# Kernel optimization log

Hardware: AMD Instinct MI355X
Metric: run time of the kernel (lower is better)

## Reference

```python
import jax, jax.numpy as jnp
import numpy as np

MAX_BOXES = 20
IOU_THRESHOLD = 0.1
SCORE_THRESHOLD = 0.3
NUM_CLASSES = 80
N_BOXES = 10647  # YOLOv3 @416: 3*(13^2 + 26^2 + 52^2)


def setup_inputs() -> dict:
    key = jax.random.key(0)
    k1, k2, k3 = jax.random.split(key, 3)
    # boxes in [y1, x1, y2, x2] format (what tf.image.non_max_suppression expects)
    mins = jax.random.uniform(k1, (N_BOXES, 2), minval=0.0, maxval=400.0)
    sizes = jax.random.uniform(k2, (N_BOXES, 2), minval=10.0, maxval=120.0)
    boxes = jnp.concatenate([mins, mins + sizes], axis=1)  # [N,4]
    box_scores = jax.random.uniform(k3, (N_BOXES, NUM_CLASSES))  # [N,C]
    return {"boxes": boxes, "box_scores": box_scores}


def _iou_one_vs_all(box, boxes):
    # box [4], boxes [N,4], format [y1,x1,y2,x2]
    tl = jnp.maximum(box[:2], boxes[:, :2])
    br = jnp.minimum(box[2:], boxes[:, 2:])
    inter = jnp.prod(jnp.clip(br - tl, 0.0), axis=1)
    area1 = jnp.prod(box[2:] - box[:2])
    areas = jnp.prod(boxes[:, 2:] - boxes[:, :2], axis=1)
    union = area1 + areas - inter
    return jnp.where(union > 0, inter / union, 0.0)


def _nms_single_class(boxes, scores):
    """Greedy NMS for one class. Returns padded ([MAX_BOXES] int32 indices, [MAX_BOXES] bool valid).
    Matches tf.image.non_max_suppression semantics (suppress when IoU > threshold),
    applied after the score_threshold mask (invalid scores set to -inf)."""
    n = scores.shape[0]
    s0 = jnp.where(scores >= SCORE_THRESHOLD, scores, -jnp.inf)

    def body(i, state):
        s, idxs, valid = state
        j = jnp.argmax(s)
        ok = s[j] > -jnp.inf
        iou = _iou_one_vs_all(boxes[j], boxes)  # [N]
        suppress = (iou > IOU_THRESHOLD) | (jnp.arange(n) == j)
        s = jnp.where(ok & suppress, -jnp.inf, s)
        idxs = idxs.at[i].set(jnp.where(ok, j, -1).astype(jnp.int32))
        valid = valid.at[i].set(ok)
        return (s, idxs, valid)

    init = (s0, jnp.full((MAX_BOXES,), -1, jnp.int32), jnp.zeros((MAX_BOXES,), bool))
    _, idxs, valid = jax.lax.fori_loop(0, MAX_BOXES, body, init)
    return idxs, valid


def reference(boxes, box_scores):
    # Per-class greedy NMS, vectorized over classes with vmap.
    idxs, valid = jax.vmap(_nms_single_class, in_axes=(None, 1))(boxes, box_scores)  # [C,MAX_BOXES]
    c = box_scores.shape[1]
    classes = jnp.broadcast_to(jnp.arange(c, dtype=jnp.int32)[:, None], (c, MAX_BOXES))
    classes = jnp.where(valid, classes, -1)
    batch_idx = jnp.where(valid, 0, -1).astype(jnp.int32)
    # Fixed-shape (padded) analogue of the variable-length concat in the original:
    # rows are [batch_index, class, box_index]; invalid slots are -1.
    nms_final = jnp.stack([batch_idx, classes, idxs], axis=-1).reshape(1, c * MAX_BOXES, 3)
    boxes_1 = boxes[None]                 # [1,N,4]
    box_scores_t_1 = box_scores.T[None]   # [1,C,N]
    return boxes_1, box_scores_t_1, nms_final
```

## Files before the change

### kernel.cpp

```cpp
#include <hip/hip_runtime.h>
#include <math.h>

#define N_BOXES 10647
#define NUM_CLASSES 80
#define MAX_BOXES 20
#define IOU_T 0.1f
#define SCORE_T 0.3f

#define NT 1024
#define NWAVES (NT / 64)
#define KP 11
#define WCAP 128
#define TGT 96

#define TROWS 64
#define TBLOCKS 167
#define CPBLOCKS 6
#define K1_BLOCKS (TBLOCKS + CPBLOCKS)

#define OUT_OFF_SCORES (N_BOXES * 4)
#define OUT_OFF_NMS (N_BOXES * 4 + NUM_CLASSES * N_BOXES)

#define FOR_K(OP) OP(0) OP(1) OP(2) OP(3) OP(4) OP(5) OP(6) OP(7) OP(8) OP(9) OP(10)

__device__ __forceinline__ bool iou_gt(float jy1, float jx1, float jy2,
                                       float jx2, float area_j, float4 b) {
    float ty = fmaxf(jy1, b.x);
    float tx = fmaxf(jx1, b.y);
    float by = fminf(jy2, b.z);
    float bx = fminf(jx2, b.w);
    float dy = fmaxf(__fsub_rn(by, ty), 0.0f);
    float dx = fmaxf(__fsub_rn(bx, tx), 0.0f);
    float inter = __fmul_rn(dy, dx);
    if (!(inter > 0.0f)) return false;
    float area_i = __fmul_rn(__fsub_rn(b.z, b.x), __fsub_rn(b.w, b.y));
    float uni = __fsub_rn(__fadd_rn(area_j, area_i), inter);
    float iou = (uni > 0.0f) ? __fdiv_rn(inter, uni) : 0.0f;
    return iou > IOU_T;
}

__global__ __launch_bounds__(NT) void transpose_copy_kernel(
    const float* __restrict__ boxes, const float* __restrict__ scores,
    float* __restrict__ out) {
    const int tid = threadIdx.x;
    const int b = blockIdx.x;

    if (b >= TBLOCKS) {
        for (int q = (b - TBLOCKS) * NT + tid; q < N_BOXES;
             q += CPBLOCKS * NT) {
            ((float4*)out)[q] = ((const float4*)boxes)[q];
        }
        return;
    }

    __shared__ float lds[TROWS * 81];
    const int r0 = b * TROWS;
    const int nr = min(TROWS, N_BOXES - r0);

    const int nq = nr * 20;
    for (int q = tid; q < nq; q += NT) {
        const int r = q / 20;
        const int c4 = (q - r * 20) * 4;
        float4 v = *(const float4*)(scores + (r0 + r) * NUM_CLASSES + c4);
        float* dst = &lds[r * 81 + c4];
        dst[0] = v.x;
        dst[1] = v.y;
        dst[2] = v.z;
        dst[3] = v.w;
    }
    __syncthreads();

    const int r = tid & (TROWS - 1);
    const int chi = tid >> 6;
    if (r < nr) {
        #pragma unroll
        for (int p = 0; p < 5; ++p) {
            const int c = p * 16 + chi;
            out[OUT_OFF_SCORES + c * N_BOXES + r0 + r] = lds[r * 81 + c];
        }
    }
}

__global__ __launch_bounds__(NT) void nms_kernel(
    const float* __restrict__ boxes, float* __restrict__ out) {
    const int tid = threadIdx.x;
    const int c = blockIdx.x;
    const int wave = tid >> 6;
    const int lane = tid & 63;
    const float4* boxes4 = (const float4*)boxes;
    const float* col = out + OUT_OFF_SCORES + c * N_BOXES;

    __shared__ int s_hist[2048];
    __shared__ unsigned long long s_k[WCAP];
    __shared__ float4 s_b4[WCAP];
    __shared__ unsigned long long s_ks[WCAP];
    __shared__ float4 s_bs[WCAP];
    __shared__ __align__(16) unsigned long long s_mask[WCAP][2];
    __shared__ unsigned long long s_rk[2][NWAVES];
    __shared__ int s_out[MAX_BOXES];
    __shared__ int s_bstar, s_total, s_cnt, s_nsel;

    if (tid < MAX_BOXES) s_out[tid] = -1;
    if (tid == 0) { s_cnt = 0; s_nsel = 0; }
    s_hist[tid] = 0;
    s_hist[tid + NT] = 0;
    __syncthreads();

#define DECL_K(k) unsigned long long k_##k = 0;
    FOR_K(DECL_K)
#undef DECL_K
#define BUILD_K(k)                                                     \
    {                                                                  \
        int i = tid + (k)*NT;                                          \
        if (i < N_BOXES) {                                             \
            float v = col[i];                                          \
            if (v >= SCORE_T) {                                        \
                unsigned int vb = __float_as_uint(v);                  \
                k_##k = ((unsigned long long)vb << 32) |               \
                        (0xFFFFFFFFu - (unsigned int)i);               \
                atomicAdd(&s_hist[(vb - 0x3E800000u) >> 13], 1);       \
            }                                                          \
        }                                                              \
    }
    FOR_K(BUILD_K)
#undef BUILD_K
    __syncthreads();

    if (wave == 0) {
        int lsum = 0;
        #pragma unroll
        for (int t = 0; t < 32; ++t) {
            int bb = (t + lane) & 31;
            lsum += s_hist[lane * 32 + bb];
        }
        int S = lsum;
        #pragma unroll
        for (int off = 1; off < 64; off <<= 1) {
            int up = __shfl_down(S, off);
            if (lane + off < 64) S += up;
        }
        unsigned long long mk = __ballot(S >= TGT);
        int bstar = 0;
        if (mk != 0) {
            const int L = 63 - __builtin_clzll(mk);
            const int S_L = __shfl(S, L);
            const int lsum_L = __shfl(lsum, L);
            const int S_above = S_L - lsum_L;
            int h = (lane < 32) ? s_hist[L * 32 + lane] : 0;
            int sfx = h;
            #pragma unroll
            for (int off = 1; off < 64; off <<= 1) {
                int up = __shfl_down(sfx, off);
                if (lane + off < 64) sfx += up;
            }
            unsigned long long sel = __ballot(sfx + S_above >= TGT);
            bstar = L * 32 + (63 - __builtin_clzll(sel));
        }
        if (lane == 0) {
            s_bstar = bstar;
            s_total = S;
        }
    }
    __syncthreads();

    const unsigned int tbits = 0x3E800000u + ((unsigned int)s_bstar << 13);

#define COMPACT_K(k)                                                    \
    {                                                                   \
        bool p = (k_##k != 0) &&                                        \
                 ((unsigned int)(k_##k >> 32) >= tbits);                \
        unsigned long long m = __ballot(p);                             \
        int basew = 0;                                                  \
        if (lane == 0 && m) basew = atomicAdd(&s_cnt, __popcll(m));     \
        basew = __shfl(basew, 0);                                       \
        if (p) {                                                        \
            int pos = basew + __popcll(m & ((1ull << lane) - 1ull));    \
            if (pos < WCAP) {                                           \
                s_k[pos] = k_##k;                                       \
                s_b4[pos] = boxes4[0xFFFFFFFFu - (unsigned int)k_##k];  \
            }                                                           \
        }                                                               \
    }
    FOR_K(COMPACT_K)
#undef COMPACT_K
    __syncthreads();

    const int wcnt = s_cnt;
    const bool overflow = (wcnt > WCAP);

    if (!overflow && tid < wcnt) {
        const unsigned long long mykey = s_k[tid];
        const float4 mybox = s_b4[tid];
        int rank = 0;
        for (int j = 0; j < wcnt; ++j) rank += (s_k[j] > mykey) ? 1 : 0;
        s_ks[rank] = mykey;
        s_bs[rank] = mybox;
    }
    __syncthreads();

    if (!overflow) {
        const int ntask = 2 * wcnt;
        for (int t = wave; t < ntask; t += NWAVES) {
            const int row = t >> 1, ch = t & 1;
            float4 rb = s_bs[row];
            float area_r =
                __fmul_rn(__fsub_rn(rb.z, rb.x), __fsub_rn(rb.w, rb.y));
            int colj = ch * 64 + lane;
            bool s = (colj < wcnt) &&
                     iou_gt(rb.x, rb.y, rb.z, rb.w, area_r, s_bs[colj]);
            unsigned long long m = __ballot(s);
            if (lane == 0) s_mask[row][ch] = m;
        }
    }
    __syncthreads();

    if (wave == 0 && !overflow) {
        unsigned long long a0, a1;
        if (wcnt >= 64) {
            a0 = ~0ull;
            a1 = (wcnt >= 128) ? ~0ull
                               : ((wcnt > 64) ? ((1ull << (wcnt - 64)) - 1)
                                              : 0ull);
        } else {
            a0 = (wcnt > 0) ? ((1ull << wcnt) - 1) : 0ull;
            a1 = 0ull;
        }
        int nkept = 0;
        while ((a0 | a1) != 0 && nkept < MAX_BOXES) {
            int pos = a0 ? __builtin_ctzll(a0)
                         : 64 + __builtin_ctzll(a1);
            if (lane == 0)
                s_out[nkept] =
                    (int)(0xFFFFFFFFu - (unsigned int)s_ks[pos]);
            ++nkept;
            ulonglong2 m = *(const ulonglong2*)&s_mask[pos][0];
            a0 &= ~m.x;
            a1 &= ~m.y;
            if (pos < 64) a0 &= ~(1ull << pos);
            else a1 &= ~(1ull << (pos - 64));
        }
        if (lane == 0) s_nsel = nkept;
    }
    __syncthreads();

    const int nsel0 = s_nsel;
    const bool needs_more =
        (nsel0 < MAX_BOXES) && (overflow || (wcnt < s_total));
    if (needs_more) {
#define LIVE_K(k)                                                        \
        if (k_##k != 0) {                                                \
            bool dead =                                                  \
                (!overflow &&                                            \
                 ((unsigned int)(k_##k >> 32) >= tbits));                \
            if (!dead && nsel0 > 0) {                                    \
                int i = tid + (k)*NT;                                    \
                float4 bi = boxes4[i];                                   \
                for (int j = 0; j < nsel0; ++j) {                        \
                    float4 sb = boxes4[s_out[j]];                        \
                    float aj = __fmul_rn(__fsub_rn(sb.z, sb.x),          \
                                         __fsub_rn(sb.w, sb.y));         \
                    if (iou_gt(sb.x, sb.y, sb.z, sb.w, aj, bi)) {        \
                        dead = true;                                     \
                        break;                                           \
                    }                                                    \
                }                                                        \
            }                                                            \
            if (dead) k_##k = 0;                                         \
        }
        FOR_K(LIVE_K)
#undef LIVE_K
        for (int slot = nsel0; slot < MAX_BOXES; ++slot) {
            unsigned long long bk = 0;
#define MAXK_K(k) if (k_##k > bk) bk = k_##k;
            FOR_K(MAXK_K)
#undef MAXK_K
            #pragma unroll
            for (int off = 32; off >= 1; off >>= 1) {
                unsigned long long o =
                    (unsigned long long)__shfl_xor((long long)bk, off);
                if (o > bk) bk = o;
            }
            const int par = slot & 1;
            if (lane == 0) s_rk[par][wave] = bk;
            __syncthreads();
            unsigned long long f = s_rk[par][0];
            #pragma unroll
            for (int w = 1; w < NWAVES; ++w) {
                unsigned long long o = s_rk[par][w];
                if (o > f) f = o;
            }
            if (f == 0) break;
            const int widx = (int)(0xFFFFFFFFu - (unsigned int)f);
            if (tid == 0) s_out[slot] = widx;
            float4 wb = boxes4[widx];
            const float area_j =
                __fmul_rn(__fsub_rn(wb.z, wb.x), __fsub_rn(wb.w, wb.y));
#define SCANE_K(k)                                                      \
            if (k_##k != 0) {                                           \
                int i = tid + (k)*NT;                                   \
                float4 b = boxes4[i];                                   \
                if (i == widx ||                                        \
                    iou_gt(wb.x, wb.y, wb.z, wb.w, area_j, b))          \
                    k_##k = 0;                                          \
            }
            FOR_K(SCANE_K)
#undef SCANE_K
        }
    }

    __syncthreads();
    if (tid < MAX_BOXES) {
        int bi = s_out[tid];
        int o = OUT_OFF_NMS + c * MAX_BOXES * 3 + tid * 3;
        if (bi >= 0) {
            out[o + 0] = 0.0f;
            out[o + 1] = (float)c;
            out[o + 2] = (float)bi;
        } else {
            out[o + 0] = -1.0f;
            out[o + 1] = -1.0f;
            out[o + 2] = -1.0f;
        }
    }
}

extern "C" void kernel_launch(void* const* d_in, const int* in_sizes, int n_in,
                              void* d_out, int out_size, void* d_ws,
                              size_t ws_size, hipStream_t stream) {
    const float* boxes = (const float*)d_in[0];
    const float* scores = (const float*)d_in[1];
    float* out = (float*)d_out;

    transpose_copy_kernel<<<K1_BLOCKS, NT, 0, stream>>>(boxes, scores, out);
    nms_kernel<<<NUM_CLASSES, NT, 0, stream>>>(boxes, out);
}
```

Before: 77.66 us.

## Fuse score transpose into NMS kernel, reading strided columns directly

Removes the separate LDS-tiled transpose kernel and has each per-class NMS block read its score column directly from the row-major input with stride NUM_CLASSES, writing the transposed column as it goes. Box copy blocks are appended to the same launch. This saves one kernel launch and the round trip through the transposed buffer. The cost is strided, uncoalesced global reads. The class-to-block mapping is swizzled so that concurrently running blocks share cache lines.

```diff
diff --git a/kernel.cpp b/kernel.cpp
--- a/kernel.cpp
+++ b/kernel.cpp
@@ -13,10 +13,7 @@
 #define WCAP 128
 #define TGT 96
 
-#define TROWS 64
-#define TBLOCKS 167
 #define CPBLOCKS 6
-#define K1_BLOCKS (TBLOCKS + CPBLOCKS)
 
 #define OUT_OFF_SCORES (N_BOXES * 4)
 #define OUT_OFF_NMS (N_BOXES * 4 + NUM_CLASSES * N_BOXES)
@@ -39,56 +36,27 @@
     return iou > IOU_T;
 }
 
-__global__ __launch_bounds__(NT) void transpose_copy_kernel(
+__global__ __launch_bounds__(NT) void fused_nms_kernel(
     const float* __restrict__ boxes, const float* __restrict__ scores,
     float* __restrict__ out) {
     const int tid = threadIdx.x;
     const int b = blockIdx.x;
 
-    if (b >= TBLOCKS) {
-        for (int q = (b - TBLOCKS) * NT + tid; q < N_BOXES;
+    if (b >= NUM_CLASSES) {
+        for (int q = (b - NUM_CLASSES) * NT + tid; q < N_BOXES;
              q += CPBLOCKS * NT) {
             ((float4*)out)[q] = ((const float4*)boxes)[q];
         }
         return;
     }
 
-    __shared__ float lds[TROWS * 81];
-    const int r0 = b * TROWS;
-    const int nr = min(TROWS, N_BOXES - r0);
-
-    const int nq = nr * 20;
-    for (int q = tid; q < nq; q += NT) {
-        const int r = q / 20;
-        const int c4 = (q - r * 20) * 4;
-        float4 v = *(const float4*)(scores + (r0 + r) * NUM_CLASSES + c4);
-        float* dst = &lds[r * 81 + c4];
-        dst[0] = v.x;
-        dst[1] = v.y;
-        dst[2] = v.z;
-        dst[3] = v.w;
-    }
-    __syncthreads();
-
-    const int r = tid & (TROWS - 1);
-    const int chi = tid >> 6;
-    if (r < nr) {
-        #pragma unroll
-        for (int p = 0; p < 5; ++p) {
-            const int c = p * 16 + chi;
-            out[OUT_OFF_SCORES + c * N_BOXES + r0 + r] = lds[r * 81 + c];
-        }
-    }
-}
-
-__global__ __launch_bounds__(NT) void nms_kernel(
-    const float* __restrict__ boxes, float* __restrict__ out) {
-    const int tid = threadIdx.x;
-    const int c = blockIdx.x;
+    const int c = (b & 7) * 10 + (b >> 3);
+
     const int wave = tid >> 6;
     const int lane = tid & 63;
     const float4* boxes4 = (const float4*)boxes;
-    const float* col = out + OUT_OFF_SCORES + c * N_BOXES;
+    const float* scol = scores + c;
+    float* tcol = out + OUT_OFF_SCORES + c * N_BOXES;
 
     __shared__ int s_hist[2048];
     __shared__ unsigned long long s_k[WCAP];
@@ -113,7 +81,8 @@
     {                                                                  \
         int i = tid + (k)*NT;                                          \
         if (i < N_BOXES) {                                             \
-            float v = col[i];                                          \
+            float v = scol[i * NUM_CLASSES];                           \
+            tcol[i] = v;                                               \
             if (v >= SCORE_T) {                                        \
                 unsigned int vb = __float_as_uint(v);                  \
                 k_##k = ((unsigned long long)vb << 32) |               \
@@ -331,6 +300,6 @@
     const float* scores = (const float*)d_in[1];
     float* out = (float*)d_out;
 
-    transpose_copy_kernel<<<K1_BLOCKS, NT, 0, stream>>>(boxes, scores, out);
-    nms_kernel<<<NUM_CLASSES, NT, 0, stream>>>(boxes, out);
+    fused_nms_kernel<<<NUM_CLASSES + CPBLOCKS, NT, 0, stream>>>(boxes, scores,
+                                                                out);
 }
```

After: 85.14 us. 9.6% more time.

## Emit high-score candidate slots from transpose kernel, replacing per-class histogram pass

Applied to the files above, without the earlier changes.

The transpose kernel now also writes, per class and per 64-row tile, up to 8 packed score/index keys for scores at or above a fixed 0.992 window threshold, with a sentinel when a tile overflows. The NMS kernel gathers these slots instead of reading the full column and building a histogram to pick a threshold, which removes the full-column scan and atomics from the common path. The fallback path now rebuilds keys from the full column only when fewer than 20 boxes are selected. This relies on the score distribution putting enough candidates above the fixed window, and it adds workspace traffic and ballot work to the transpose.

```diff
diff --git a/kernel.cpp b/kernel.cpp
--- a/kernel.cpp
+++ b/kernel.cpp
@@ -7,16 +7,20 @@
 #define IOU_T 0.1f
 #define SCORE_T 0.3f
 
+#define WND_T 0.992f
+
 #define NT 1024
 #define NWAVES (NT / 64)
-#define KP 11
 #define WCAP 128
-#define TGT 96
 
 #define TROWS 64
 #define TBLOCKS 167
 #define CPBLOCKS 6
 #define K1_BLOCKS (TBLOCKS + CPBLOCKS)
+
+#define WSLOTS 8
+#define SLOT_N (TBLOCKS * WSLOTS)
+#define SENTINEL (~0ull)
 
 #define OUT_OFF_SCORES (N_BOXES * 4)
 #define OUT_OFF_NMS (N_BOXES * 4 + NUM_CLASSES * N_BOXES)
@@ -39,9 +43,9 @@
     return iou > IOU_T;
 }
 
-__global__ __launch_bounds__(NT) void transpose_copy_kernel(
+__global__ __launch_bounds__(NT) void transpose_slots_kernel(
     const float* __restrict__ boxes, const float* __restrict__ scores,
-    float* __restrict__ out) {
+    float* __restrict__ out, unsigned long long* __restrict__ ws) {
     const int tid = threadIdx.x;
     const int b = blockIdx.x;
 
@@ -72,17 +76,37 @@
 
     const int r = tid & (TROWS - 1);
     const int chi = tid >> 6;
-    if (r < nr) {
-        #pragma unroll
-        for (int p = 0; p < 5; ++p) {
-            const int c = p * 16 + chi;
-            out[OUT_OFF_SCORES + c * N_BOXES + r0 + r] = lds[r * 81 + c];
+    #pragma unroll
+    for (int p = 0; p < 5; ++p) {
+        const int c = p * 16 + chi;
+        float v = 0.0f;
+        if (r < nr) {
+            v = lds[r * 81 + c];
+            out[OUT_OFF_SCORES + c * N_BOXES + r0 + r] = v;
+        }
+        const bool cand = (r < nr) && (v >= WND_T);
+        const unsigned long long mask = __ballot(cand);
+        unsigned long long* slot = ws + ((size_t)c * TBLOCKS + b) * WSLOTS;
+        const int cnt = __popcll(mask);
+        if (cnt <= WSLOTS) {
+            if (cand) {
+                const int rank =
+                    __popcll(mask & ((1ull << r) - 1ull));
+                slot[rank] =
+                    ((unsigned long long)__float_as_uint(v) << 32) |
+                    (0xFFFFFFFFu - (unsigned)(r0 + r));
+            }
+            if (r >= cnt && r < WSLOTS) slot[r] = 0ull;
+        } else {
+            if (r == 0) slot[0] = SENTINEL;
+            if (r >= 1 && r < WSLOTS) slot[r] = 0ull;
         }
     }
 }
 
 __global__ __launch_bounds__(NT) void nms_kernel(
-    const float* __restrict__ boxes, float* __restrict__ out) {
+    const float* __restrict__ boxes, float* __restrict__ out,
+    const unsigned long long* __restrict__ ws) {
     const int tid = threadIdx.x;
     const int c = blockIdx.x;
     const int wave = tid >> 6;
@@ -90,7 +114,6 @@
     const float4* boxes4 = (const float4*)boxes;
     const float* col = out + OUT_OFF_SCORES + c * N_BOXES;
 
-    __shared__ int s_hist[2048];
     __shared__ unsigned long long s_k[WCAP];
     __shared__ float4 s_b4[WCAP];
     __shared__ unsigned long long s_ks[WCAP];
@@ -98,95 +121,39 @@
     __shared__ __align__(16) unsigned long long s_mask[WCAP][2];
     __shared__ unsigned long long s_rk[2][NWAVES];
     __shared__ int s_out[MAX_BOXES];
-    __shared__ int s_bstar, s_total, s_cnt, s_nsel;
+    __shared__ int s_cnt, s_nsel, s_ovf;
 
     if (tid < MAX_BOXES) s_out[tid] = -1;
-    if (tid == 0) { s_cnt = 0; s_nsel = 0; }
-    s_hist[tid] = 0;
-    s_hist[tid + NT] = 0;
-    __syncthreads();
-
-#define DECL_K(k) unsigned long long k_##k = 0;
-    FOR_K(DECL_K)
-#undef DECL_K
-#define BUILD_K(k)                                                     \
-    {                                                                  \
-        int i = tid + (k)*NT;                                          \
-        if (i < N_BOXES) {                                             \
-            float v = col[i];                                          \
-            if (v >= SCORE_T) {                                        \
-                unsigned int vb = __float_as_uint(v);                  \
-                k_##k = ((unsigned long long)vb << 32) |               \
-                        (0xFFFFFFFFu - (unsigned int)i);               \
-                atomicAdd(&s_hist[(vb - 0x3E800000u) >> 13], 1);       \
-            }                                                          \
-        }                                                              \
-    }
-    FOR_K(BUILD_K)
-#undef BUILD_K
-    __syncthreads();
-
-    if (wave == 0) {
-        int lsum = 0;
-        #pragma unroll
-        for (int t = 0; t < 32; ++t) {
-            int bb = (t + lane) & 31;
-            lsum += s_hist[lane * 32 + bb];
-        }
-        int S = lsum;
-        #pragma unroll
-        for (int off = 1; off < 64; off <<= 1) {
-            int up = __shfl_down(S, off);
-            if (lane + off < 64) S += up;
-        }
-        unsigned long long mk = __ballot(S >= TGT);
-        int bstar = 0;
-        if (mk != 0) {
-            const int L = 63 - __builtin_clzll(mk);
-            const int S_L = __shfl(S, L);
-            const int lsum_L = __shfl(lsum, L);
-            const int S_above = S_L - lsum_L;
-            int h = (lane < 32) ? s_hist[L * 32 + lane] : 0;
-            int sfx = h;
-            #pragma unroll
-            for (int off = 1; off < 64; off <<= 1) {
-                int up = __shfl_down(sfx, off);
-                if (lane + off < 64) sfx += up;
-            }
-            unsigned long long sel = __ballot(sfx + S_above >= TGT);
-            bstar = L * 32 + (63 - __builtin_clzll(sel));
-        }
-        if (lane == 0) {
-            s_bstar = bstar;
-            s_total = S;
-        }
-    }
-    __syncthreads();
-
-    const unsigned int tbits = 0x3E800000u + ((unsigned int)s_bstar << 13);
-
-#define COMPACT_K(k)                                                    \
-    {                                                                   \
-        bool p = (k_##k != 0) &&                                        \
-                 ((unsigned int)(k_##k >> 32) >= tbits);                \
-        unsigned long long m = __ballot(p);                             \
-        int basew = 0;                                                  \
-        if (lane == 0 && m) basew = atomicAdd(&s_cnt, __popcll(m));     \
-        basew = __shfl(basew, 0);                                       \
-        if (p) {                                                        \
-            int pos = basew + __popcll(m & ((1ull << lane) - 1ull));    \
-            if (pos < WCAP) {                                           \
-                s_k[pos] = k_##k;                                       \
-                s_b4[pos] = boxes4[0xFFFFFFFFu - (unsigned int)k_##k];  \
-            }                                                           \
-        }                                                               \
-    }
-    FOR_K(COMPACT_K)
-#undef COMPACT_K
+    if (tid == 0) { s_cnt = 0; s_nsel = 0; s_ovf = 0; }
+    __syncthreads();
+
+    const unsigned long long* wsl = ws + (size_t)c * SLOT_N;
+    for (int q = tid; q < SLOT_N; q += NT) {
+        unsigned long long s = wsl[q];
+        bool val = false;
+        if (s != 0ull) {
+            if ((unsigned)(s >> 32) >= 0x3F800000u) {
+                s_ovf = 1;
+            } else {
+                val = true;
+            }
+        }
+        const unsigned long long m = __ballot(val);
+        int basew = 0;
+        if (lane == 0 && m) basew = atomicAdd(&s_cnt, __popcll(m));
+        basew = __shfl(basew, 0);
+        if (val) {
+            const int pos = basew + __popcll(m & ((1ull << lane) - 1ull));
+            if (pos < WCAP) {
+                s_k[pos] = s;
+                s_b4[pos] = boxes4[0xFFFFFFFFu - (unsigned)s];
+            }
+        }
+    }
     __syncthreads();
 
     const int wcnt = s_cnt;
-    const bool overflow = (wcnt > WCAP);
+    const bool overflow = (wcnt > WCAP) || (s_ovf != 0);
 
     if (!overflow && tid < wcnt) {
         const unsigned long long mykey = s_k[tid];
@@ -244,31 +211,41 @@
     __syncthreads();
 
     const int nsel0 = s_nsel;
-    const bool needs_more =
-        (nsel0 < MAX_BOXES) && (overflow || (wcnt < s_total));
+    const bool needs_more = (nsel0 < MAX_BOXES);
     if (needs_more) {
-#define LIVE_K(k)                                                        \
-        if (k_##k != 0) {                                                \
-            bool dead =                                                  \
-                (!overflow &&                                            \
-                 ((unsigned int)(k_##k >> 32) >= tbits));                \
-            if (!dead && nsel0 > 0) {                                    \
-                int i = tid + (k)*NT;                                    \
-                float4 bi = boxes4[i];                                   \
-                for (int j = 0; j < nsel0; ++j) {                        \
-                    float4 sb = boxes4[s_out[j]];                        \
-                    float aj = __fmul_rn(__fsub_rn(sb.z, sb.x),          \
-                                         __fsub_rn(sb.w, sb.y));         \
-                    if (iou_gt(sb.x, sb.y, sb.z, sb.w, aj, bi)) {        \
-                        dead = true;                                     \
-                        break;                                           \
+#define DECL_K(k) unsigned long long k_##k = 0;
+        FOR_K(DECL_K)
+#undef DECL_K
+#define BUILDE_K(k)                                                      \
+        {                                                                \
+            int i = tid + (k)*NT;                                        \
+            if (i < N_BOXES) {                                           \
+                float v = col[i];                                        \
+                if (v >= SCORE_T) {                                      \
+                    bool dead = (!overflow && v >= WND_T);               \
+                    if (!dead && nsel0 > 0) {                            \
+                        float4 bi = boxes4[i];                           \
+                        for (int j = 0; j < nsel0; ++j) {                \
+                            float4 sb = boxes4[s_out[j]];                \
+                            float aj =                                   \
+                                __fmul_rn(__fsub_rn(sb.z, sb.x),         \
+                                          __fsub_rn(sb.w, sb.y));        \
+                            if (iou_gt(sb.x, sb.y, sb.z, sb.w, aj,       \
+                                       bi)) {                            \
+                                dead = true;                             \
+                                break;                                   \
+                            }                                            \
+                        }                                                \
                     }                                                    \
+                    if (!dead)                                           \
+                        k_##k = ((unsigned long long)__float_as_uint(v)  \
+                                 << 32) |                                \
+                                (0xFFFFFFFFu - (unsigned int)i);         \
                 }                                                        \
             }                                                            \
-            if (dead) k_##k = 0;                                         \
-        }
-        FOR_K(LIVE_K)
-#undef LIVE_K
+        }
+        FOR_K(BUILDE_K)
+#undef BUILDE_K
         for (int slot = nsel0; slot < MAX_BOXES; ++slot) {
             unsigned long long bk = 0;
 #define MAXK_K(k) if (k_##k > bk) bk = k_##k;
@@ -330,7 +307,9 @@
     const float* boxes = (const float*)d_in[0];
     const float* scores = (const float*)d_in[1];
     float* out = (float*)d_out;
-
-    transpose_copy_kernel<<<K1_BLOCKS, NT, 0, stream>>>(boxes, scores, out);
-    nms_kernel<<<NUM_CLASSES, NT, 0, stream>>>(boxes, out);
+    unsigned long long* ws = (unsigned long long*)d_ws;
+
+    transpose_slots_kernel<<<K1_BLOCKS, NT, 0, stream>>>(boxes, scores, out,
+                                                         ws);
+    nms_kernel<<<NUM_CLASSES, NT, 0, stream>>>(boxes, out, ws);
 }
```

New measurement: 71.33 us. 8.2% less time.
